# Kernel tuning notes

Measured on AMD Instinct MI355X. Metric: run time of the kernel, lower is better.

Reference implementation:

```python
import jax, jax.numpy as jnp
import numpy as np

D, C, H, W = 8, 512, 64, 64


def setup_inputs() -> dict:
    key = jax.random.key(0)
    k1, k2, k3 = jax.random.split(key, 3)
    x = jax.random.normal(k1, (D, C, H, W), dtype=jnp.float32)
    atten = jax.random.normal(k2, (D, C, C), dtype=jnp.float32)
    gamma = jax.random.normal(k3, (1,), dtype=jnp.float32)
    return {"x": x, "atten": atten, "gamma": gamma}


def reference(x, atten, gamma):
    d, c, h, w = x.shape
    q = x.reshape(d, c, h * w)              # q == v == flattened x; k = q^T
    # energy[d, i, j] = <channel_i, channel_j> over spatial positions
    energy = jnp.einsum('din,djn->dij', q, q)
    # max-centering: rowmax - energy (note the sign flip vs standard softmax)
    energy_new = jnp.max(energy, axis=-1, keepdims=True) - energy
    attention = jax.nn.softmax(energy_new, axis=-1)
    attention = jax.nn.softmax(attention + atten, axis=-1)
    # out = attention^T @ v : out[d, j, n] = sum_i attention[d, i, j] * v[d, i, n]
    out = jnp.einsum('dij,din->djn', attention, q).reshape(d, c, h, w)
    return gamma * out + x
```

## Files before the change

kernel.cpp:

```cpp
#include <hip/hip_runtime.h>
#include <hip/hip_bf16.h>

#define DD 8
#define CC 512
#define NN 4096

typedef __bf16 bf16x8 __attribute__((ext_vector_type(8)));
typedef float  f32x4  __attribute__((ext_vector_type(4)));
typedef ushort ush8   __attribute__((ext_vector_type(8)));

__device__ __forceinline__ ushort f2bf(float f) {
  unsigned u = __float_as_uint(f);
  u = (u + 0x7fffu + ((u >> 16) & 1u)) >> 16;
  return (ushort)u;
}
__device__ __forceinline__ float bf2f(ushort h) {
  return __uint_as_float(((unsigned)h) << 16);
}

__device__ __forceinline__ void gl_lds16(const ushort* g, ushort* l) {
  __builtin_amdgcn_global_load_lds(
      (const __attribute__((address_space(1))) void*)g,
      (__attribute__((address_space(3))) void*)l, 16, 0, 0);
}


__global__ __launch_bounds__(256) void k0_convert(
    const float* __restrict__ x, ushort* __restrict__ qh,
    ushort* __restrict__ ql, ushort* __restrict__ qt) {
  int d = blockIdx.z, ct = blockIdx.y, nt = blockIdx.x;
  __shared__ ushort T[64][68];
  int t = threadIdx.x;
  int rr = t >> 4;
  int c4 = (t & 15) * 4;
  const float* xb = x + ((size_t)(d * CC + ct * 64)) * NN + nt * 64;
#pragma unroll
  for (int it = 0; it < 4; ++it) {
    int r = it * 16 + rr;
    float4 v = *(const float4*)(xb + (size_t)r * NN + c4);
    ushort h0 = f2bf(v.x), h1 = f2bf(v.y), h2 = f2bf(v.z), h3 = f2bf(v.w);
    ushort l0 = f2bf(v.x - bf2f(h0)), l1 = f2bf(v.y - bf2f(h1));
    ushort l2 = f2bf(v.z - bf2f(h2)), l3 = f2bf(v.w - bf2f(h3));
    size_t qi = ((size_t)(d * CC + ct * 64 + r)) * NN + nt * 64 + c4;
    *(ushort4*)(qh + qi) = make_ushort4(h0, h1, h2, h3);
    *(ushort4*)(ql + qi) = make_ushort4(l0, l1, l2, l3);
    *(ushort4*)&T[r][c4] = make_ushort4(h0, h1, h2, h3);
  }
  __syncthreads();
#pragma unroll
  for (int it = 0; it < 4; ++it) {
    int nl = it * 16 + rr;
    ushort4 v = make_ushort4(T[c4 + 0][nl], T[c4 + 1][nl], T[c4 + 2][nl], T[c4 + 3][nl]);
    *(ushort4*)(qt + ((size_t)(d * NN + nt * 64 + nl)) * CC + ct * 64 + c4) = v;
  }
}

#define K1_STAGE(S)                                                            \
  {                                                                            \
    ushort* ls = lbase + ((S) & 1) * 8192;                                     \
    const ushort* gs = gsrc + (size_t)(S) * 32;                                \
    _Pragma("unroll")                                                          \
    for (int c = 0; c < 8; ++c)                                                \
      gl_lds16(gs + (size_t)c * 16 * NN, ls + c * 512);                        \
  }

#define K1_COMPUTE(SOFF)                                                       \
  {                                                                            \
    bf16x8 ah[4], al[4];                                                       \
    _Pragma("unroll")                                                          \
    for (int mi = 0; mi < 4; ++mi) {                                           \
      int off = (SOFF) + (wm + mi * 16 + fr) * 32 + qo;                        \
      ah[mi] = *(const bf16x8*)&As[off];                                       \
      al[mi] = *(const bf16x8*)&As[off + 4096];                                \
    }                                                                          \
    _Pragma("unroll")                                                          \
    for (int ni = 0; ni < 4; ++ni) {                                           \
      int off = (SOFF) + (wn + ni * 16 + fr) * 32 + qo;                        \
      bf16x8 bh = *(const bf16x8*)&Bs[off];                                    \
      bf16x8 bl = *(const bf16x8*)&Bs[off + 4096];                             \
      _Pragma("unroll")                                                        \
      for (int mi = 0; mi < 4; ++mi) {                                         \
        acc[mi][ni] = __builtin_amdgcn_mfma_f32_16x16x32_bf16(ah[mi], bh, acc[mi][ni], 0, 0, 0); \
        acc[mi][ni] = __builtin_amdgcn_mfma_f32_16x16x32_bf16(ah[mi], bl, acc[mi][ni], 0, 0, 0); \
        acc[mi][ni] = __builtin_amdgcn_mfma_f32_16x16x32_bf16(al[mi], bh, acc[mi][ni], 0, 0, 0); \
      }                                                                        \
    }                                                                          \
  }

__global__ __launch_bounds__(256, 2) void k1_gram(
    const ushort* __restrict__ qh, const ushort* __restrict__ ql,
    float* __restrict__ Ep, int ns, int nkk, int ksp) {
  __shared__ ushort As[2 * 2 * 4096];
  __shared__ ushort Bs[2 * 2 * 4096];
  int b = blockIdx.x;
  int s = b % ns;
  int rem = b / ns;
  int tile = rem % 10, d = rem / 10;
  int tm = (int)((0x3221110000ULL >> (tile * 4)) & 15ULL);
  int tn = (int)((0x3323213210ULL >> (tile * 4)) & 15ULL);
  int t = threadIdx.x, lane = t & 63, w = t >> 6;
  int wm = (w >> 1) * 64, wn = (w & 1) * 64;
  int qd = lane >> 4, fr = lane & 15;
  int qo = (qd ^ ((fr >> 1) & 3)) * 8;
  int so = ((lane & 3) ^ ((lane >> 3) & 3)) * 8;

  const ushort* srcbase = (w & 1) ? ql : qh;
  int rowblk = (w < 2) ? tm : tn;
  const ushort* gsrc = srcbase +
      ((size_t)(d * CC + rowblk * 128 + (lane >> 2))) * NN +
      (size_t)s * ksp + so;
  ushort* lbase = ((w < 2) ? As : Bs) + (w & 1) * 4096;

  f32x4 acc[4][4];
#pragma unroll
  for (int i = 0; i < 4; ++i)
#pragma unroll
    for (int j = 0; j < 4; ++j) acc[i][j] = (f32x4){0.f, 0.f, 0.f, 0.f};

  K1_STAGE(0)

#pragma unroll 1
  for (int kk = 0; kk < nkk - 1; ++kk) {
    asm volatile("s_waitcnt lgkmcnt(0)\n\ts_barrier" ::: "memory");
    K1_STAGE(kk + 1)
    asm volatile("s_waitcnt vmcnt(8)\n\ts_barrier" ::: "memory");
    K1_COMPUTE((kk & 1) * 8192)
  }
  asm volatile("s_waitcnt vmcnt(0) lgkmcnt(0)\n\ts_barrier" ::: "memory");
  K1_COMPUTE(((nkk - 1) & 1) * 8192)

  size_t ebase = ((size_t)(s * DD + d)) * ((size_t)CC * CC);
#pragma unroll
  for (int mi = 0; mi < 4; ++mi) {
    int r0 = tm * 128 + wm + mi * 16 + qd * 4;
#pragma unroll
    for (int ni = 0; ni < 4; ++ni) {
      int c0 = tn * 128 + wn + ni * 16 + fr;
      float* ep = Ep + ebase + (size_t)r0 * CC + c0;
#pragma unroll
      for (int r = 0; r < 4; ++r) ep[(size_t)r * CC] = acc[mi][ni][r];
    }
  }
  if (tm != tn) {
#pragma unroll
    for (int mi = 0; mi < 4; ++mi) {
      int r0 = tm * 128 + wm + mi * 16 + qd * 4;
#pragma unroll
      for (int ni = 0; ni < 4; ++ni) {
        int c0 = tn * 128 + wn + ni * 16 + fr;
        float4 v = make_float4(acc[mi][ni][0], acc[mi][ni][1],
                               acc[mi][ni][2], acc[mi][ni][3]);
        *(float4*)(Ep + ebase + (size_t)c0 * CC + r0) = v;
      }
    }
  }
}

__device__ __forceinline__ float wmin(float v) {
#pragma unroll
  for (int o = 32; o > 0; o >>= 1) v = fminf(v, __shfl_xor(v, o));
  return v;
}
__device__ __forceinline__ float wmax(float v) {
#pragma unroll
  for (int o = 32; o > 0; o >>= 1) v = fmaxf(v, __shfl_xor(v, o));
  return v;
}
__device__ __forceinline__ float wsum(float v) {
#pragma unroll
  for (int o = 32; o > 0; o >>= 1) v += __shfl_xor(v, o);
  return v;
}

__global__ __launch_bounds__(256) void k2_softmax(
    const float* __restrict__ Ep, const float* __restrict__ atten,
    ushort* __restrict__ a2t, int ns) {
  int d = blockIdx.y, i0 = blockIdx.x * 8;
  int t = threadIdx.x, lane = t & 63, w = t >> 6;
  int j8 = lane * 8;
  __shared__ ushort T[8][520];
  const size_t SP = (size_t)DD * CC * CC;

#pragma unroll
  for (int r2 = 0; r2 < 2; ++r2) {
    int ri = w * 2 + r2;
    size_t base = ((size_t)(d * CC + i0 + ri)) * CC + j8;
    f32x4 a0 = (f32x4){0.f, 0.f, 0.f, 0.f};
    f32x4 a1 = (f32x4){0.f, 0.f, 0.f, 0.f};
    for (int s = 0; s < ns; ++s) {
      const float* p = Ep + (size_t)s * SP + base;
      a0 += *(const f32x4*)p;
      a1 += *(const f32x4*)(p + 4);
    }
    float mn = fminf(fminf(fminf(a0[0], a0[1]), fminf(a0[2], a0[3])),
                     fminf(fminf(a1[0], a1[1]), fminf(a1[2], a1[3])));
    mn = wmin(mn);
    float p0 = __expf(mn - a0[0]), p1 = __expf(mn - a0[1]);
    float p2 = __expf(mn - a0[2]), p3 = __expf(mn - a0[3]);
    float p4 = __expf(mn - a1[0]), p5 = __expf(mn - a1[1]);
    float p6 = __expf(mn - a1[2]), p7 = __expf(mn - a1[3]);
    float s1 = wsum(p0 + p1 + p2 + p3 + p4 + p5 + p6 + p7);
    float inv1 = 1.0f / s1;
    const float* ap = atten + base;
    f32x4 t0 = *(const f32x4*)ap;
    f32x4 t1 = *(const f32x4*)(ap + 4);
    float u0 = p0 * inv1 + t0[0], u1 = p1 * inv1 + t0[1];
    float u2 = p2 * inv1 + t0[2], u3 = p3 * inv1 + t0[3];
    float u4 = p4 * inv1 + t1[0], u5 = p5 * inv1 + t1[1];
    float u6 = p6 * inv1 + t1[2], u7 = p7 * inv1 + t1[3];
    float mx = wmax(fmaxf(fmaxf(fmaxf(u0, u1), fmaxf(u2, u3)),
                          fmaxf(fmaxf(u4, u5), fmaxf(u6, u7))));
    float q0 = __expf(u0 - mx), q1 = __expf(u1 - mx);
    float q2 = __expf(u2 - mx), q3 = __expf(u3 - mx);
    float q4 = __expf(u4 - mx), q5 = __expf(u5 - mx);
    float q6 = __expf(u6 - mx), q7 = __expf(u7 - mx);
    float s2 = wsum(q0 + q1 + q2 + q3 + q4 + q5 + q6 + q7);
    float inv2 = 1.0f / s2;
    ush8 o;
    o[0] = f2bf(q0 * inv2); o[1] = f2bf(q1 * inv2);
    o[2] = f2bf(q2 * inv2); o[3] = f2bf(q3 * inv2);
    o[4] = f2bf(q4 * inv2); o[5] = f2bf(q5 * inv2);
    o[6] = f2bf(q6 * inv2); o[7] = f2bf(q7 * inv2);
    *(ush8*)&T[ri][j8] = o;
  }
  __syncthreads();
#pragma unroll
  for (int it = 0; it < 2; ++it) {
    int j = t + it * 256;
    ush8 o;
#pragma unroll
    for (int k = 0; k < 8; ++k) o[k] = T[k][j];
    *(ush8*)&a2t[((size_t)(d * CC + j)) * CC + i0] = o;
  }
}

#define K3_COMPUTE(SOFF)                                                       \
  {                                                                            \
    bf16x8 qf[4];                                                              \
    _Pragma("unroll")                                                          \
    for (int ii = 0; ii < 4; ++ii)                                             \
      qf[ii] = *(const bf16x8*)&Bs[(SOFF) + (wn2 + ii * 16 + fr) * 32 + qo];   \
    _Pragma("unroll")                                                          \
    for (int jj = 0; jj < 4; ++jj) {                                           \
      bf16x8 af = *(const bf16x8*)&As[(SOFF) + (wj + jj * 16 + fr) * 32 + qo]; \
      _Pragma("unroll")                                                        \
      for (int ii = 0; ii < 4; ++ii)                                           \
        acc[ii][jj] = __builtin_amdgcn_mfma_f32_16x16x32_bf16(                 \
            qf[ii], af, acc[ii][jj], 0, 0, 0);                                 \
    }                                                                          \
  }

#define K3_STAGE(S)                                                            \
  {                                                                            \
    ushort* ls = mylds + ((S) & 3) * 4096;                                     \
    const ushort* gs = g0 + (size_t)(S) * 32;                                  \
    _Pragma("unroll")                                                          \
    for (int c = 0; c < 4; ++c)                                                \
      gl_lds16(gs + (size_t)(c * 16) * CC, ls + c * 512);                      \
  }

__global__ __launch_bounds__(256, 2) void k3_out(
    const ushort* __restrict__ a2t, const ushort* __restrict__ qt,
    const float* __restrict__ x, const float* __restrict__ gamma,
    float* __restrict__ out, int d0) {
  __shared__ ushort As[4 * 128 * 32];
  __shared__ ushort Bs[4 * 128 * 32];
  int b = blockIdx.x;
  int nt = b & 31, jt = (b >> 5) & 3, d = d0 + (b >> 7);
  int t = threadIdx.x, lane = t & 63, w = t >> 6;
  int wj = (w >> 1) * 64, wn2 = (w & 1) * 64;
  int qd = lane >> 4, fr = lane & 15;
  int qo = (qd ^ ((fr >> 1) & 3)) * 8;
  int so = ((lane & 3) ^ ((lane >> 3) & 3)) * 8;

  const ushort* src = (w < 2)
      ? (a2t + (size_t)d * CC * CC + (size_t)(jt * 128) * CC)
      : (qt + (size_t)d * NN * CC + (size_t)(nt * 128) * CC);
  int cbase = (w & 1) * 4;
  const ushort* g0 = src + ((size_t)(cbase * 16 + (lane >> 2))) * CC + so;
  ushort* mylds = ((w < 2) ? As : Bs) + cbase * 512;

  f32x4 acc[4][4];
#pragma unroll
  for (int i = 0; i < 4; ++i)
#pragma unroll
    for (int j = 0; j < 4; ++j) acc[i][j] = (f32x4){0.f, 0.f, 0.f, 0.f};

  K3_STAGE(0)
  K3_STAGE(1)
  K3_STAGE(2)

#pragma unroll 1
  for (int kk = 0; kk < 13; ++kk) {
    asm volatile("s_waitcnt vmcnt(8)\n\ts_barrier" ::: "memory");
    K3_STAGE(kk + 3)
    K3_COMPUTE((kk & 3) * 4096)
  }
  asm volatile("s_waitcnt vmcnt(8)\n\ts_barrier" ::: "memory");
  K3_COMPUTE(1 * 4096)
  asm volatile("s_waitcnt vmcnt(4)\n\ts_barrier" ::: "memory");
  K3_COMPUTE(2 * 4096)
  asm volatile("s_waitcnt vmcnt(0)\n\ts_barrier" ::: "memory");

  int n0b = nt * 128 + wn2 + qd * 4;
  float4 xp0[4], xp1[4];
#pragma unroll
  for (int jj = 0; jj < 4; ++jj) {
    size_t rb = ((size_t)(d * CC + jt * 128 + wj + jj * 16 + fr)) * NN;
    xp0[jj] = *(const float4*)(x + rb + n0b);
    xp1[jj] = *(const float4*)(x + rb + n0b + 16);
  }
  K3_COMPUTE(3 * 4096)

  float g = gamma[0];
  float4 x2[4], x3[4];
#pragma unroll
  for (int jj = 0; jj < 4; ++jj)
    x2[jj] = *(const float4*)(x + ((size_t)(d * CC + jt * 128 + wj + jj * 16 + fr)) * NN + n0b + 32);
#pragma unroll
  for (int jj = 0; jj < 4; ++jj) {
    size_t idx = ((size_t)(d * CC + jt * 128 + wj + jj * 16 + fr)) * NN + n0b;
    *(float4*)(out + idx) = make_float4(g * acc[0][jj][0] + xp0[jj].x,
                                        g * acc[0][jj][1] + xp0[jj].y,
                                        g * acc[0][jj][2] + xp0[jj].z,
                                        g * acc[0][jj][3] + xp0[jj].w);
  }
#pragma unroll
  for (int jj = 0; jj < 4; ++jj)
    x3[jj] = *(const float4*)(x + ((size_t)(d * CC + jt * 128 + wj + jj * 16 + fr)) * NN + n0b + 48);
#pragma unroll
  for (int jj = 0; jj < 4; ++jj) {
    size_t idx = ((size_t)(d * CC + jt * 128 + wj + jj * 16 + fr)) * NN + n0b + 16;
    *(float4*)(out + idx) = make_float4(g * acc[1][jj][0] + xp1[jj].x,
                                        g * acc[1][jj][1] + xp1[jj].y,
                                        g * acc[1][jj][2] + xp1[jj].z,
                                        g * acc[1][jj][3] + xp1[jj].w);
  }
#pragma unroll
  for (int jj = 0; jj < 4; ++jj) {
    size_t idx = ((size_t)(d * CC + jt * 128 + wj + jj * 16 + fr)) * NN + n0b + 32;
    *(float4*)(out + idx) = make_float4(g * acc[2][jj][0] + x2[jj].x,
                                        g * acc[2][jj][1] + x2[jj].y,
                                        g * acc[2][jj][2] + x2[jj].z,
                                        g * acc[2][jj][3] + x2[jj].w);
  }
#pragma unroll
  for (int jj = 0; jj < 4; ++jj) {
    size_t idx = ((size_t)(d * CC + jt * 128 + wj + jj * 16 + fr)) * NN + n0b + 48;
    *(float4*)(out + idx) = make_float4(g * acc[3][jj][0] + x3[jj].x,
                                        g * acc[3][jj][1] + x3[jj].y,
                                        g * acc[3][jj][2] + x3[jj].z,
                                        g * acc[3][jj][3] + x3[jj].w);
  }
}

extern "C" void kernel_launch(void* const* d_in, const int* in_sizes, int n_in,
                              void* d_out, int out_size, void* d_ws, size_t ws_size,
                              hipStream_t stream) {
  (void)in_sizes; (void)n_in; (void)out_size;
  const float* x     = (const float*)d_in[0];
  const float* atten = (const float*)d_in[1];
  const float* gamma = (const float*)d_in[2];
  float* out = (float*)d_out;

  char* ws = (char*)d_ws;
  ushort* qh  = (ushort*)(ws);
  ushort* ql  = (ushort*)(ws + 33554432);
  ushort* qt  = (ushort*)(ws + 67108864);
  ushort* a2t = (ushort*)(ws + 100663296);
  float*  Ep  = (float*) (ws + 104857600);

  int ns = (ws_size >= 104857600ULL + 8ULL * 8388608ULL) ? 8 : 4;
  int ksp = NN / ns;
  int nkk = ksp / 32;

  k0_convert<<<dim3(64, 8, 8), 256, 0, stream>>>(x, qh, ql, qt);
  k1_gram   <<<dim3(80 * ns), 256, 0, stream>>>(qh, ql, Ep, ns, nkk, ksp);
  k2_softmax<<<dim3(64, 8), 256, 0, stream>>>(Ep, atten, a2t, ns);
  k3_out    <<<dim3(512), 256, 0, stream>>>(a2t, qt, x, gamma, out, 0);
  k3_out    <<<dim3(512), 256, 0, stream>>>(a2t, qt, x, gamma, out, 4);
}
```

Before: 239.9 us.

## Reduce split-K Gram partials with atomics into a single zeroed buffer

Replaces the per-split partial energy buffers, which were summed in the softmax kernel, with float atomicAdd into one shared Ep buffer that the convert kernel zeroes first. This removes writing and reading eight partial matrices per batch, cutting DRAM traffic for the reduction. In exchange the Gram epilogue issues many scalar atomics (the transposed store loses its float4 vectorization), which adds atomic contention, and the summation order becomes nondeterministic.

```diff
diff --git a/kernel.cpp b/kernel.cpp
--- a/kernel.cpp
+++ b/kernel.cpp
@@ -27,10 +27,14 @@
 
 __global__ __launch_bounds__(256) void k0_convert(
     const float* __restrict__ x, ushort* __restrict__ qh,
-    ushort* __restrict__ ql, ushort* __restrict__ qt) {
+    ushort* __restrict__ ql, ushort* __restrict__ qt,
+    float* __restrict__ Ep) {
   int d = blockIdx.z, ct = blockIdx.y, nt = blockIdx.x;
   __shared__ ushort T[64][68];
   int t = threadIdx.x;
+  size_t fid = ((((size_t)blockIdx.z * 8 + blockIdx.y) * 64 + blockIdx.x) * 256 + t) * 2;
+  *(float2*)(Ep + fid) = make_float2(0.f, 0.f);
+
   int rr = t >> 4;
   int c4 = (t & 15) * 4;
   const float* xb = x + ((size_t)(d * CC + ct * 64)) * NN + nt * 64;
@@ -129,7 +133,7 @@
   asm volatile("s_waitcnt vmcnt(0) lgkmcnt(0)\n\ts_barrier" ::: "memory");
   K1_COMPUTE(((nkk - 1) & 1) * 8192)
 
-  size_t ebase = ((size_t)(s * DD + d)) * ((size_t)CC * CC);
+  size_t ebase = (size_t)d * ((size_t)CC * CC);
 #pragma unroll
   for (int mi = 0; mi < 4; ++mi) {
     int r0 = tm * 128 + wm + mi * 16 + qd * 4;
@@ -138,7 +142,7 @@
       int c0 = tn * 128 + wn + ni * 16 + fr;
       float* ep = Ep + ebase + (size_t)r0 * CC + c0;
 #pragma unroll
-      for (int r = 0; r < 4; ++r) ep[(size_t)r * CC] = acc[mi][ni][r];
+      for (int r = 0; r < 4; ++r) atomicAdd(ep + (size_t)r * CC, acc[mi][ni][r]);
     }
   }
   if (tm != tn) {
@@ -148,9 +152,11 @@
 #pragma unroll
       for (int ni = 0; ni < 4; ++ni) {
         int c0 = tn * 128 + wn + ni * 16 + fr;
-        float4 v = make_float4(acc[mi][ni][0], acc[mi][ni][1],
-                               acc[mi][ni][2], acc[mi][ni][3]);
-        *(float4*)(Ep + ebase + (size_t)c0 * CC + r0) = v;
+        float* mp = Ep + ebase + (size_t)c0 * CC + r0;
+        atomicAdd(mp + 0, acc[mi][ni][0]);
+        atomicAdd(mp + 1, acc[mi][ni][1]);
+        atomicAdd(mp + 2, acc[mi][ni][2]);
+        atomicAdd(mp + 3, acc[mi][ni][3]);
       }
     }
   }
@@ -174,24 +180,19 @@
 
 __global__ __launch_bounds__(256) void k2_softmax(
     const float* __restrict__ Ep, const float* __restrict__ atten,
-    ushort* __restrict__ a2t, int ns) {
+    ushort* __restrict__ a2t) {
   int d = blockIdx.y, i0 = blockIdx.x * 8;
   int t = threadIdx.x, lane = t & 63, w = t >> 6;
   int j8 = lane * 8;
   __shared__ ushort T[8][520];
-  const size_t SP = (size_t)DD * CC * CC;
 
 #pragma unroll
   for (int r2 = 0; r2 < 2; ++r2) {
     int ri = w * 2 + r2;
     size_t base = ((size_t)(d * CC + i0 + ri)) * CC + j8;
-    f32x4 a0 = (f32x4){0.f, 0.f, 0.f, 0.f};
-    f32x4 a1 = (f32x4){0.f, 0.f, 0.f, 0.f};
-    for (int s = 0; s < ns; ++s) {
-      const float* p = Ep + (size_t)s * SP + base;
-      a0 += *(const f32x4*)p;
-      a1 += *(const f32x4*)(p + 4);
-    }
+    const float* p = Ep + base;
+    f32x4 a0 = *(const f32x4*)p;
+    f32x4 a1 = *(const f32x4*)(p + 4);
     float mn = fminf(fminf(fminf(a0[0], a0[1]), fminf(a0[2], a0[3])),
                      fminf(fminf(a1[0], a1[1]), fminf(a1[2], a1[3])));
     mn = wmin(mn);
@@ -357,7 +358,7 @@
 extern "C" void kernel_launch(void* const* d_in, const int* in_sizes, int n_in,
                               void* d_out, int out_size, void* d_ws, size_t ws_size,
                               hipStream_t stream) {
-  (void)in_sizes; (void)n_in; (void)out_size;
+  (void)in_sizes; (void)n_in; (void)out_size; (void)ws_size;
   const float* x     = (const float*)d_in[0];
   const float* atten = (const float*)d_in[1];
   const float* gamma = (const float*)d_in[2];
@@ -370,13 +371,13 @@
   ushort* a2t = (ushort*)(ws + 100663296);
   float*  Ep  = (float*) (ws + 104857600);
 
-  int ns = (ws_size >= 104857600ULL + 8ULL * 8388608ULL) ? 8 : 4;
-  int ksp = NN / ns;
-  int nkk = ksp / 32;
-
-  k0_convert<<<dim3(64, 8, 8), 256, 0, stream>>>(x, qh, ql, qt);
+  const int ns = 8;
+  const int ksp = NN / ns;
+  const int nkk = ksp / 32;
+
+  k0_convert<<<dim3(64, 8, 8), 256, 0, stream>>>(x, qh, ql, qt, Ep);
   k1_gram   <<<dim3(80 * ns), 256, 0, stream>>>(qh, ql, Ep, ns, nkk, ksp);
-  k2_softmax<<<dim3(64, 8), 256, 0, stream>>>(Ep, atten, a2t, ns);
+  k2_softmax<<<dim3(64, 8), 256, 0, stream>>>(Ep, atten, a2t);
   k3_out    <<<dim3(512), 256, 0, stream>>>(a2t, qt, x, gamma, out, 0);
   k3_out    <<<dim3(512), 256, 0, stream>>>(a2t, qt, x, gamma, out, 4);
 }
```

Result: slower. 314.1 us (+30.9%).
